# Kernel tuning notes

Measured on AMD Instinct MI355X. Metric: run time of the kernel, lower is better.

Reference implementation:

```python
import jax, jax.numpy as jnp
import numpy as np

DIM = 1024
DIM_HEAD = 64
S = 8   # num_searches
R = 2   # num_retrievals
B = 2
N = 2048


def setup_inputs() -> dict:
    key = jax.random.key(0)
    ks = jax.random.split(key, 7)
    wscale = 1.0 / np.sqrt(DIM)
    return {
        "x": jax.random.normal(ks[0], (B, N, DIM), dtype=jnp.float32),
        "Wsq": jax.random.normal(ks[1], (DIM, S * DIM_HEAD), dtype=jnp.float32) * wscale,
        "Wsk": jax.random.normal(ks[2], (DIM, S * DIM_HEAD), dtype=jnp.float32) * wscale,
        "Wrv": jax.random.normal(ks[3], (DIM, R * DIM_HEAD), dtype=jnp.float32) * wscale,
        "Wrq": jax.random.normal(ks[4], (DIM, S * DIM_HEAD), dtype=jnp.float32) * wscale,
        "Wrk": jax.random.normal(ks[5], (DIM_HEAD, DIM_HEAD), dtype=jnp.float32) * (1.0 / np.sqrt(DIM_HEAD)),
        "Wout": jax.random.normal(ks[6], (S * DIM_HEAD, DIM), dtype=jnp.float32) * (1.0 / np.sqrt(S * DIM_HEAD)),
    }


def reference(x, Wsq, Wsk, Wrv, Wrq, Wrk, Wout):
    b, n, _ = x.shape
    d = DIM_HEAD
    scale = d ** -0.5

    # search queries/keys: [b, s, n, d]
    sq = (x @ Wsq).reshape(b, n, S, d).transpose(0, 2, 1, 3)
    sk = (x @ Wsk).reshape(b, n, S, d).transpose(0, 2, 1, 3)

    # search attention over sequence: [b, s, n, n]
    sim = jnp.einsum('bsid,bsjd->bsij', sq, sk) * scale
    attn = jax.nn.softmax(sim, axis=-1)

    # retrieval values: [b, r, n, d]
    v = (x @ Wrv).reshape(b, n, R, d).transpose(0, 2, 1, 3)

    # each search retrieves with every retrieval value set: [b, s, r, n, d]
    retrieved = jnp.einsum('bsij,brjd->bsrid', attn, v)

    # retrieval queries [b, s, n, d] and transformed retrieval keys [b, s, r, n, d]
    rq = (x @ Wrq).reshape(b, n, S, d).transpose(0, 2, 1, 3)
    rk = jnp.einsum('bsrnd,de->bsrne', retrieved, Wrk)

    # compositional softmax over retrievals: [b, s, n, r]
    r_sim = jnp.einsum('bsnd,bsrnd->bsnr', rq, rk) * scale
    r_attn = jax.nn.softmax(r_sim, axis=-1)

    # combine: [b, s, n, d] -> [b, n, s*d]
    out = jnp.einsum('bsnr,bsrnd->bsnd', r_attn, retrieved)
    out = out.transpose(0, 2, 1, 3).reshape(b, n, S * d)
    return out @ Wout
```

## Files before the change

### kernel.cpp

```cpp
#include <hip/hip_runtime.h>

#define NSEQ 2048
#define KDIM 1024
#define DH   64
#define NS   8
#define NR   2

typedef short bf16x8 __attribute__((ext_vector_type(8)));
typedef float f32x4  __attribute__((ext_vector_type(4)));

typedef unsigned short ushort_ma __attribute__((may_alias));
typedef bf16x8         bf16x8_ma __attribute__((may_alias));
typedef uint4          uint4_ma  __attribute__((may_alias));
typedef uint2          uint2_ma  __attribute__((may_alias));
typedef float4         float4_ma __attribute__((may_alias));

__device__ __forceinline__ unsigned short f2bf(float f) {
    unsigned int u = __builtin_bit_cast(unsigned int, f);
    u = (u + 0x7FFFu + ((u >> 16) & 1u)) >> 16;
    return (unsigned short)u;
}
__device__ __forceinline__ float bf2f(unsigned short h) {
    unsigned int u = ((unsigned int)h) << 16;
    return __builtin_bit_cast(float, u);
}
__device__ __forceinline__ unsigned int cvt_pk_bf16(float lo, float hi) {
    unsigned int r;
    asm("v_cvt_pk_bf16_f32 %0, %1, %2" : "=v"(r) : "v"(lo), "v"(hi));
    return r;
}
__device__ __forceinline__ float exp2_raw(float x) {
    return __builtin_amdgcn_exp2f(x);
}
__device__ __forceinline__ void gld_lds16(void* lptr, const void* gptr) {
    __builtin_amdgcn_global_load_lds(
        (const __attribute__((address_space(1))) unsigned int*)gptr,
        (__attribute__((address_space(3))) unsigned int*)lptr, 16, 0, 0);
}

__global__ __launch_bounds__(256) void prep_all_k(
    const float* __restrict__ Wsq, const float* __restrict__ Wsk,
    const float* __restrict__ Wrq, const float* __restrict__ Wrv,
    const float* __restrict__ Wout, const float* __restrict__ Wrk,
    const float* __restrict__ x,
    unsigned short* __restrict__ Wt, unsigned short* __restrict__ Wot,
    unsigned short* __restrict__ xh)
{
    __shared__ float sBuf[2][64][65];
    const int tid = threadIdx.x;
    const int bid = blockIdx.x;

    if (bid >= 672) {
        const int total = 4096 * KDIM / 4;
        int idx = (bid - 672) * 256 + tid;
        for (int i = idx; i < total; i += 2048 * 256) {
            float4 v = ((const float4_ma*)x)[i];
            ushort4 h;
            h.x = f2bf(v.x); h.y = f2bf(v.y); h.z = f2bf(v.z); h.w = f2bf(v.w);
            ((ushort4*)xh)[i] = h;
        }
        return;
    }

    if (bid >= 544) {
        const int r = bid - 544;
        const int s = r & 7;
        const int k0 = (r >> 3) * 64;
        float (*sQ)[65] = sBuf[0];
        float (*sK)[65] = sBuf[1];
#pragma unroll
        for (int p = 0; p < 4; ++p) {
            int row = (tid >> 4) + p * 16;
            int col = (tid & 15) * 4;
            float4 w = *(const float4*)&Wrk[(size_t)row * 64 + col];
            sK[row][col + 0] = w.x; sK[row][col + 1] = w.y;
            sK[row][col + 2] = w.z; sK[row][col + 3] = w.w;
            float4 q = *(const float4*)&Wrq[(size_t)(k0 + row) * 512 + s * 64 + col];
            sQ[row][col + 0] = q.x; sQ[row][col + 1] = q.y;
            sQ[row][col + 2] = q.z; sQ[row][col + 3] = q.w;
        }
        __syncthreads();

        const int dd = tid >> 2;
        const int kq = (tid & 3) * 16;
        float acc[16];
#pragma unroll
        for (int j = 0; j < 16; ++j) acc[j] = 0.f;
        for (int e = 0; e < 64; ++e) {
            float w = sK[dd][e];
#pragma unroll
            for (int j = 0; j < 16; ++j) acc[j] += w * sQ[kq + j][e];
        }
        const float SC = 0.125f * 1.44269504089f;
        unsigned int w8[8];
#pragma unroll
        for (int j = 0; j < 8; ++j)
            w8[j] = (unsigned)f2bf(acc[2 * j] * SC) | ((unsigned)f2bf(acc[2 * j + 1] * SC) << 16);
        unsigned short* o = Wt + (size_t)(1024 + s * 64 + dd) * KDIM + k0 + kq;
        *(uint4_ma*)o       = make_uint4(w8[0], w8[1], w8[2], w8[3]);
        *(uint4_ma*)(o + 8) = make_uint4(w8[4], w8[5], w8[6], w8[7]);
        return;
    }

    {
        const float* src; int ldw, k0, n0, scol, ldo;
        unsigned short* dst;
        float sc = 1.0f;
        if (bid < 416) {
            int kt = bid / 26, nt = bid % 26;
            k0 = kt * 64; n0 = nt * 64;
            if (n0 >= 1024 && n0 < 1536) return;
            if (n0 < 512)       { src = Wsq; ldw = 512; scol = n0;        sc = 0.125f * 1.44269504089f; }
            else if (n0 < 1024) { src = Wsk; ldw = 512; scol = n0 - 512;  }
            else                { src = Wrv; ldw = 128; scol = n0 - 1536; }
            dst = Wt; ldo = KDIM;
        } else {
            int r = bid - 416;
            int kt = r >> 4, nt = r & 15;
            k0 = kt * 64; n0 = nt * 64; scol = n0;
            src = Wout; ldw = KDIM;
            dst = Wot; ldo = 512;
        }
        float (*sT)[65] = sBuf[0];
#pragma unroll
        for (int p = 0; p < 4; ++p) {
            int row = (tid >> 4) + p * 16;
            int col = (tid & 15) * 4;
            float4 v = *(const float4*)&src[(size_t)(k0 + row) * ldw + scol + col];
            sT[row][col + 0] = v.x; sT[row][col + 1] = v.y;
            sT[row][col + 2] = v.z; sT[row][col + 3] = v.w;
        }
        __syncthreads();

        int n_l = tid >> 2, kg = (tid & 3) * 16;
        unsigned int w[8];
#pragma unroll
        for (int j = 0; j < 8; ++j) {
            unsigned short a = f2bf(sT[kg + 2 * j][n_l] * sc);
            unsigned short b = f2bf(sT[kg + 2 * j + 1][n_l] * sc);
            w[j] = (unsigned)a | ((unsigned)b << 16);
        }
        unsigned short* o = dst + (size_t)(n0 + n_l) * ldo + k0 + kg;
        *(uint4_ma*)o       = make_uint4(w[0], w[1], w[2], w[3]);
        *(uint4_ma*)(o + 8) = make_uint4(w[4], w[5], w[6], w[7]);
    }
}

__global__ __launch_bounds__(256) void proj_mfma_k(
    const unsigned short* __restrict__ xh,
    const unsigned short* __restrict__ Wt,
    unsigned short* __restrict__ Qb, unsigned short* __restrict__ Kf,
    unsigned short* __restrict__ RUb, unsigned short* __restrict__ Vf)
{
    __shared__ __align__(16) char smem[32768];
    const int tid = threadIdx.x;
    const int bn = blockIdx.x, bm = blockIdx.y;
    const int wid = tid >> 6, lane = tid & 63;
    const int wm = wid >> 1, wn = wid & 1;
    const int lrow = lane & 15, lgrp = lane >> 4;
    const int lr = lane >> 3, lc = lane & 7;

    f32x4 acc[4][4];
#pragma unroll
    for (int i = 0; i < 4; ++i)
#pragma unroll
        for (int j = 0; j < 4; ++j) acc[i][j] = (f32x4){0.f, 0.f, 0.f, 0.f};

    for (int kt = 0; kt < KDIM / 64; ++kt) {
        __syncthreads();
#pragma unroll
        for (int i = 0; i < 4; ++i) {
            int seg = wid * 4 + i;
            int r = seg * 8 + lr;
            gld_lds16(smem + seg * 1024,
                      xh + (size_t)(bm * 128 + r) * KDIM + kt * 64 + (lc ^ (r & 7)) * 8);
            gld_lds16(smem + 16384 + seg * 1024,
                      Wt + (size_t)(bn * 128 + r) * KDIM + kt * 64 + (lc ^ (r & 7)) * 8);
        }
        __syncthreads();
#pragma unroll
        for (int ks = 0; ks < 2; ++ks) {
            bf16x8 bfr[4];
#pragma unroll
            for (int nf = 0; nf < 4; ++nf) {
                int rb = wn * 64 + nf * 16 + lrow;
                bfr[nf] = *(bf16x8_ma*)(smem + 16384 + ((rb * 128 + ks * 64 + lgrp * 16) ^ ((rb & 7) << 4)));
            }
#pragma unroll
            for (int mf = 0; mf < 4; ++mf) {
                int ra = wm * 64 + mf * 16 + lrow;
                bf16x8 ah = *(bf16x8_ma*)(smem + ((ra * 128 + ks * 64 + lgrp * 16) ^ ((ra & 7) << 4)));
#pragma unroll
                for (int nf = 0; nf < 4; ++nf)
                    acc[mf][nf] = __builtin_amdgcn_mfma_f32_16x16x32_bf16(ah, bfr[nf], acc[mf][nf], 0, 0, 0);
            }
        }
    }

    const int g = bn >> 2;
#pragma unroll
    for (int mf = 0; mf < 4; ++mf) {
#pragma unroll
        for (int nf = 0; nf < 4; ++nf) {
            int j0 = bn * 128 + wn * 64 + nf * 16 + lrow;
            int m0 = bm * 128 + wm * 64 + mf * 16 + lgrp * 4;
            if (g == 3) {
                int dv = j0 - 1536;
                int bb = m0 >> 11, seq = m0 & (NSEQ - 1);
                size_t addr = (size_t)bb * 262144 + (size_t)(seq >> 6) * 8192
                    + (size_t)(((dv >> 4) * 2 + ((seq >> 5) & 1)) * 512)
                    + (((seq >> 3) & 3) * 16 + (dv & 15)) * 8 + (seq & 7);
                ushort4 h;
                h.x = f2bf(acc[mf][nf][0]); h.y = f2bf(acc[mf][nf][1]);
                h.z = f2bf(acc[mf][nf][2]); h.w = f2bf(acc[mf][nf][3]);
                *(ushort4*)&Vf[addr] = h;
            } else if (g == 1) {
                int s = (j0 >> 6) & 7, d = j0 & 63;
#pragma unroll
                for (int r = 0; r < 4; ++r) {
                    int m = m0 + r;
                    int bb = m >> 11, seq = m & (NSEQ - 1);
                    size_t base = ((size_t)(bb * NS + s)) * (NSEQ * DH)
                        + (size_t)(seq >> 6) * 4096
                        + ((((seq >> 4) & 3) * 2 + (d >> 5)) * 64
                           + ((d & 31) >> 3) * 16 + (seq & 15)) * 8 + (d & 7);
                    Kf[base] = f2bf(acc[mf][nf][r]);
                }
            } else {
                int s = (j0 >> 6) & 7, d = j0 & 63;
                unsigned short* basep = (g == 0) ? Qb : RUb;
#pragma unroll
                for (int r = 0; r < 4; ++r) {
                    int m = m0 + r;
                    int bb = m >> 11, seq = m & (NSEQ - 1);
                    basep[(((size_t)(bb * NS + s)) * NSEQ + seq) * DH + d] = f2bf(acc[mf][nf][r]);
                }
            }
        }
    }
}

__global__ __launch_bounds__(256) void attn_mfma_k(
    const unsigned short* __restrict__ Qb, const unsigned short* __restrict__ Kfr,
    const unsigned short* __restrict__ Vfr, const unsigned short* __restrict__ RUb,
    unsigned short* __restrict__ O1b)
{
    __shared__ __align__(16) char smem[8192];
    const int tid = threadIdx.x;
    const int gblk = blockIdx.x;
    const int orig = ((gblk & 7) << 6) + (gblk >> 3);
    const int qt = orig & 31, s = (orig >> 5) & 7, b = orig >> 8;
    const int wid = tid >> 6, lane = tid & 63;
    const int lrow = lane & 15, lgrp = lane >> 4;

    const unsigned short* Qg = Qb + (((size_t)(b * NS + s)) * NSEQ + qt * 64) * DH;
    const unsigned short* kp0 = Kfr + ((size_t)(b * NS + s)) * (NSEQ * DH) + lane * 8;
    const unsigned short* kp1 = kp0 + 2048;
    const unsigned short* vp0 = Vfr + (size_t)b * 262144 + lane * 8;
    const unsigned short* vp1 = vp0 + 2048;
    const unsigned short* vp2 = vp0 + 4096;
    const unsigned short* vp3 = vp0 + 6144;

    bf16x8 qf[2];
    {
        const unsigned short* qrow = Qg + (wid * 16 + lrow) * DH + lgrp * 8;
        qf[0] = *(const bf16x8_ma*)(qrow);
        qf[1] = *(const bf16x8_ma*)(qrow + 32);
    }

    char* sPw = smem + wid * 2048;
    const int pswz = (lrow & 7) << 4;

    bf16x8 kf[8], vf[16];
#define LOADK() do {                                                          \
        kf[0] = *(const bf16x8_ma*)(kp0);                                     \
        kf[1] = *(const bf16x8_ma*)(kp0 + 512);                               \
        kf[2] = *(const bf16x8_ma*)(kp0 + 1024);                              \
        kf[3] = *(const bf16x8_ma*)(kp0 + 1536);                              \
        kf[4] = *(const bf16x8_ma*)(kp1);                                     \
        kf[5] = *(const bf16x8_ma*)(kp1 + 512);                               \
        kf[6] = *(const bf16x8_ma*)(kp1 + 1024);                              \
        kf[7] = *(const bf16x8_ma*)(kp1 + 1536);                              \
        kp0 += 4096; kp1 += 4096;                                             \
    } while (0)
#define LOADV() do {                                                          \
        _Pragma("unroll")                                                     \
        for (int i_ = 0; i_ < 4; ++i_) {                                      \
            vf[i_]      = *(const bf16x8_ma*)(vp0 + i_ * 512);                \
            vf[4 + i_]  = *(const bf16x8_ma*)(vp1 + i_ * 512);                \
            vf[8 + i_]  = *(const bf16x8_ma*)(vp2 + i_ * 512);                \
            vf[12 + i_] = *(const bf16x8_ma*)(vp3 + i_ * 512);                \
        }                                                                     \
        vp0 += 8192; vp1 += 8192; vp2 += 8192; vp3 += 8192;                   \
    } while (0)

    f32x4 oacc[8];
#pragma unroll
    for (int df = 0; df < 8; ++df) oacc[df] = (f32x4){0.f, 0.f, 0.f, 0.f};
    float l_ = 0.f;
    f32x4 st[4];

    const int NT = NSEQ / 64;
    LOADK();

    for (int t = 0; t < NT; ++t) {
        LOADV();

        __builtin_amdgcn_s_setprio(1);
#pragma unroll
        for (int nf = 0; nf < 4; ++nf) {
            st[nf] = (f32x4){0.f, 0.f, 0.f, 0.f};
            st[nf] = __builtin_amdgcn_mfma_f32_16x16x32_bf16(kf[nf * 2],     qf[0], st[nf], 0, 0, 0);
            st[nf] = __builtin_amdgcn_mfma_f32_16x16x32_bf16(kf[nf * 2 + 1], qf[1], st[nf], 0, 0, 0);
        }
        __builtin_amdgcn_s_setprio(0);

        LOADK();

        float rs = 0.f;
#pragma unroll
        for (int nf = 0; nf < 4; ++nf)
#pragma unroll
            for (int r = 0; r < 4; ++r) {
                float p = exp2_raw(st[nf][r]);
                st[nf][r] = p;
                rs += p;
            }
        l_ += rs;

#pragma unroll
        for (int nf = 0; nf < 4; ++nf) {
            uint2 w;
            w.x = cvt_pk_bf16(st[nf][0], st[nf][1]);
            w.y = cvt_pk_bf16(st[nf][2], st[nf][3]);
            *(uint2_ma*)(sPw + ((lrow * 128 + nf * 32 + lgrp * 8) ^ pswz)) = w;
        }

        __builtin_amdgcn_s_setprio(1);
#pragma unroll
        for (int kkv = 0; kkv < 2; ++kkv) {
            bf16x8 pf = *(bf16x8_ma*)(sPw + ((lrow * 128 + kkv * 64 + lgrp * 16) ^ pswz));
#pragma unroll
            for (int df = 0; df < 8; ++df)
                oacc[df] = __builtin_amdgcn_mfma_f32_16x16x32_bf16(vf[df * 2 + kkv], pf, oacc[df], 0, 0, 0);
        }
        __builtin_amdgcn_s_setprio(0);
    }
#undef LOADK
#undef LOADV

    l_ += __shfl_xor(l_, 16);
    l_ += __shfl_xor(l_, 32);

    {
        const int n = qt * 64 + wid * 16 + lrow;
        const unsigned short* ug = RUb + ((((size_t)(b * NS + s)) * NSEQ) + n) * DH + lgrp * 4;
        float s0 = 0.f, s1 = 0.f;
#pragma unroll
        for (int df = 0; df < 4; ++df) {
            ushort4 u4 = *(const ushort4*)(ug + df * 16);
            float ux = bf2f(u4.x), uy = bf2f(u4.y), uz = bf2f(u4.z), uw = bf2f(u4.w);
            s0 += oacc[df][0] * ux + oacc[df][1] * uy + oacc[df][2] * uz + oacc[df][3] * uw;
            s1 += oacc[df + 4][0] * ux + oacc[df + 4][1] * uy + oacc[df + 4][2] * uz + oacc[df + 4][3] * uw;
        }
        s0 += __shfl_xor(s0, 16); s0 += __shfl_xor(s0, 32);
        s1 += __shfl_xor(s1, 16); s1 += __shfl_xor(s1, 32);
        float invl = 1.f / l_;
        float r0v = s0 * invl, r1v = s1 * invl;
        float mm = fmaxf(r0v, r1v);
        float e0 = exp2_raw(r0v - mm), e1 = exp2_raw(r1v - mm);
        float w = invl / (e0 + e1);
        float a0 = e0 * w, a1 = e1 * w;

        unsigned short* dst = O1b + ((size_t)(b * NSEQ + n)) * (NS * DH) + s * DH + lgrp * 4;
#pragma unroll
        for (int df = 0; df < 4; ++df) {
            float c0 = a0 * oacc[df][0] + a1 * oacc[df + 4][0];
            float c1 = a0 * oacc[df][1] + a1 * oacc[df + 4][1];
            float c2 = a0 * oacc[df][2] + a1 * oacc[df + 4][2];
            float c3 = a0 * oacc[df][3] + a1 * oacc[df + 4][3];
            uint2 o2;
            o2.x = cvt_pk_bf16(c0, c1);
            o2.y = cvt_pk_bf16(c2, c3);
            *(uint2_ma*)(dst + df * 16) = o2;
        }
    }
}

__global__ __launch_bounds__(256) void out_mfma_k(
    const unsigned short* __restrict__ A, const unsigned short* __restrict__ Bw,
    float* __restrict__ C)
{
    __shared__ __align__(16) char smem[32768];
    const int tid = threadIdx.x;
    const int bn = blockIdx.x, bm = blockIdx.y;
    const int wid = tid >> 6, lane = tid & 63;
    const int wm = wid >> 1, wn = wid & 1;
    const int lrow = lane & 15, lgrp = lane >> 4;
    const int lr = lane >> 3, lc = lane & 7;
    const int KD = NS * DH;

    f32x4 acc[4][4];
#pragma unroll
    for (int i = 0; i < 4; ++i)
#pragma unroll
        for (int j = 0; j < 4; ++j) acc[i][j] = (f32x4){0.f, 0.f, 0.f, 0.f};

    for (int kt = 0; kt < KD / 64; ++kt) {
        __syncthreads();
#pragma unroll
        for (int i = 0; i < 4; ++i) {
            int seg = wid * 4 + i;
            int r = seg * 8 + lr;
            gld_lds16(smem + seg * 1024,
                      A + (size_t)(bm * 128 + r) * KD + kt * 64 + (lc ^ (r & 7)) * 8);
            gld_lds16(smem + 16384 + seg * 1024,
                      Bw + (size_t)(bn * 128 + r) * KD + kt * 64 + (lc ^ (r & 7)) * 8);
        }
        __syncthreads();
#pragma unroll
        for (int ks = 0; ks < 2; ++ks) {
            bf16x8 bfr[4];
#pragma unroll
            for (int nf = 0; nf < 4; ++nf) {
                int rb = wn * 64 + nf * 16 + lrow;
                bfr[nf] = *(bf16x8_ma*)(smem + 16384 + ((rb * 128 + ks * 64 + lgrp * 16) ^ ((rb & 7) << 4)));
            }
#pragma unroll
            for (int mf = 0; mf < 4; ++mf) {
                int ra = wm * 64 + mf * 16 + lrow;
                bf16x8 af = *(bf16x8_ma*)(smem + ((ra * 128 + ks * 64 + lgrp * 16) ^ ((ra & 7) << 4)));
#pragma unroll
                for (int nf = 0; nf < 4; ++nf)
                    acc[mf][nf] = __builtin_amdgcn_mfma_f32_16x16x32_bf16(af, bfr[nf], acc[mf][nf], 0, 0, 0);
            }
        }
    }

#pragma unroll
    for (int mf = 0; mf < 4; ++mf) {
#pragma unroll
        for (int nf = 0; nf < 4; ++nf) {
            int j0 = bn * 128 + wn * 64 + nf * 16 + lrow;
            int m0 = bm * 128 + wm * 64 + mf * 16 + lgrp * 4;
#pragma unroll
            for (int r = 0; r < 4; ++r)
                C[(size_t)(m0 + r) * KDIM + j0] = acc[mf][nf][r];
        }
    }
}

extern "C" void kernel_launch(void* const* d_in, const int* in_sizes, int n_in,
                              void* d_out, int out_size, void* d_ws, size_t ws_size,
                              hipStream_t stream)
{
    const float* x    = (const float*)d_in[0];
    const float* Wsq  = (const float*)d_in[1];
    const float* Wsk  = (const float*)d_in[2];
    const float* Wrv  = (const float*)d_in[3];
    const float* Wrq  = (const float*)d_in[4];
    const float* Wrk  = (const float*)d_in[5];
    const float* Wout = (const float*)d_in[6];
    float* out = (float*)d_out;

    unsigned short* RUb  = (unsigned short*)d_ws;
    unsigned short* Wt   = RUb + (size_t)2 * NS * NSEQ * DH;
    unsigned short* Wot  = Wt + (size_t)1664 * KDIM;
    unsigned short* Qb   = Wot + (size_t)KDIM * 512;
    unsigned short* Kfr  = Qb + (size_t)2 * NS * NSEQ * DH;
    unsigned short* Vfr  = Kfr + (size_t)2 * NS * NSEQ * DH;
    unsigned short* xh   = Vfr + (size_t)2 * 128 * NSEQ;
    unsigned short* O1b  = xh;

    prep_all_k<<<2720, 256, 0, stream>>>(Wsq, Wsk, Wrq, Wrv, Wout, Wrk, x, Wt, Wot, xh);
    proj_mfma_k<<<dim3(13, 32), 256, 0, stream>>>(xh, Wt, Qb, Kfr, RUb, Vfr);
    attn_mfma_k<<<512, 256, 0, stream>>>(Qb, Kfr, Vfr, RUb, O1b);
    out_mfma_k<<<dim3(8, 32), 256, 0, stream>>>(O1b, Wot, out);
}
```

Before: 107.0 us.

## Prefetch K and V tiles with inline-asm global loads and manual vmcnt waits

Replaces the compiler-generated K/V fragment loads in the attention loop with inline-asm global_load_dwordx4 and explicit s_waitcnt vmcnt counters. V for the next tile is now issued right after the PV MFMAs, so the V fetch overlaps the following QK MFMAs and softmax instead of stalling at the start of each tile. Sched barriers pin the ordering. The risk is that asm volatile loads hide dependencies from the compiler, and any wrong vmcnt count gives a data race. The extra in-flight registers may also lower occupancy.

```diff
diff --git a/kernel.cpp b/kernel.cpp
--- a/kernel.cpp
+++ b/kernel.cpp
@@ -272,27 +272,40 @@
     const int pswz = (lrow & 7) << 4;
 
     bf16x8 kf[8], vf[16];
-#define LOADK() do {                                                          \
-        kf[0] = *(const bf16x8_ma*)(kp0);                                     \
-        kf[1] = *(const bf16x8_ma*)(kp0 + 512);                               \
-        kf[2] = *(const bf16x8_ma*)(kp0 + 1024);                              \
-        kf[3] = *(const bf16x8_ma*)(kp0 + 1536);                              \
-        kf[4] = *(const bf16x8_ma*)(kp1);                                     \
-        kf[5] = *(const bf16x8_ma*)(kp1 + 512);                               \
-        kf[6] = *(const bf16x8_ma*)(kp1 + 1024);                              \
-        kf[7] = *(const bf16x8_ma*)(kp1 + 1536);                              \
-        kp0 += 4096; kp1 += 4096;                                             \
-    } while (0)
-#define LOADV() do {                                                          \
-        _Pragma("unroll")                                                     \
-        for (int i_ = 0; i_ < 4; ++i_) {                                      \
-            vf[i_]      = *(const bf16x8_ma*)(vp0 + i_ * 512);                \
-            vf[4 + i_]  = *(const bf16x8_ma*)(vp1 + i_ * 512);                \
-            vf[8 + i_]  = *(const bf16x8_ma*)(vp2 + i_ * 512);                \
-            vf[12 + i_] = *(const bf16x8_ma*)(vp3 + i_ * 512);                \
-        }                                                                     \
-        vp0 += 8192; vp1 += 8192; vp2 += 8192; vp3 += 8192;                   \
-    } while (0)
+#define LOADK_ASM() do {                                                              \
+    asm volatile("global_load_dwordx4 %0, %1, off"             : "=&v"(kf[0]) : "v"(kp0)); \
+    asm volatile("global_load_dwordx4 %0, %1, off offset:1024" : "=&v"(kf[1]) : "v"(kp0)); \
+    asm volatile("global_load_dwordx4 %0, %1, off offset:2048" : "=&v"(kf[2]) : "v"(kp0)); \
+    asm volatile("global_load_dwordx4 %0, %1, off offset:3072" : "=&v"(kf[3]) : "v"(kp0)); \
+    asm volatile("global_load_dwordx4 %0, %1, off"             : "=&v"(kf[4]) : "v"(kp1)); \
+    asm volatile("global_load_dwordx4 %0, %1, off offset:1024" : "=&v"(kf[5]) : "v"(kp1)); \
+    asm volatile("global_load_dwordx4 %0, %1, off offset:2048" : "=&v"(kf[6]) : "v"(kp1)); \
+    asm volatile("global_load_dwordx4 %0, %1, off offset:3072" : "=&v"(kf[7]) : "v"(kp1)); \
+    kp0 += 4096; kp1 += 4096;                                                         \
+} while (0)
+#define LOADV_ASM() do {                                                              \
+    asm volatile("global_load_dwordx4 %0, %1, off"             : "=&v"(vf[0])  : "v"(vp0)); \
+    asm volatile("global_load_dwordx4 %0, %1, off offset:1024" : "=&v"(vf[1])  : "v"(vp0)); \
+    asm volatile("global_load_dwordx4 %0, %1, off offset:2048" : "=&v"(vf[2])  : "v"(vp0)); \
+    asm volatile("global_load_dwordx4 %0, %1, off offset:3072" : "=&v"(vf[3])  : "v"(vp0)); \
+    asm volatile("global_load_dwordx4 %0, %1, off"             : "=&v"(vf[4])  : "v"(vp1)); \
+    asm volatile("global_load_dwordx4 %0, %1, off offset:1024" : "=&v"(vf[5])  : "v"(vp1)); \
+    asm volatile("global_load_dwordx4 %0, %1, off offset:2048" : "=&v"(vf[6])  : "v"(vp1)); \
+    asm volatile("global_load_dwordx4 %0, %1, off offset:3072" : "=&v"(vf[7])  : "v"(vp1)); \
+    asm volatile("global_load_dwordx4 %0, %1, off"             : "=&v"(vf[8])  : "v"(vp2)); \
+    asm volatile("global_load_dwordx4 %0, %1, off offset:1024" : "=&v"(vf[9])  : "v"(vp2)); \
+    asm volatile("global_load_dwordx4 %0, %1, off offset:2048" : "=&v"(vf[10]) : "v"(vp2)); \
+    asm volatile("global_load_dwordx4 %0, %1, off offset:3072" : "=&v"(vf[11]) : "v"(vp2)); \
+    asm volatile("global_load_dwordx4 %0, %1, off"             : "=&v"(vf[12]) : "v"(vp3)); \
+    asm volatile("global_load_dwordx4 %0, %1, off offset:1024" : "=&v"(vf[13]) : "v"(vp3)); \
+    asm volatile("global_load_dwordx4 %0, %1, off offset:2048" : "=&v"(vf[14]) : "v"(vp3)); \
+    asm volatile("global_load_dwordx4 %0, %1, off offset:3072" : "=&v"(vf[15]) : "v"(vp3)); \
+    vp0 += 8192; vp1 += 8192; vp2 += 8192; vp3 += 8192;                               \
+} while (0)
+#define WAITCNT(N) do {                                                       \
+    asm volatile("s_waitcnt vmcnt(" #N ")" ::: "memory");                     \
+    __builtin_amdgcn_sched_barrier(0);                                        \
+} while (0)
 
     f32x4 oacc[8];
 #pragma unroll
@@ -301,10 +314,11 @@
     f32x4 st[4];
 
     const int NT = NSEQ / 64;
-    LOADK();
+    LOADK_ASM();
+    LOADV_ASM();
 
     for (int t = 0; t < NT; ++t) {
-        LOADV();
+        WAITCNT(16);
 
         __builtin_amdgcn_s_setprio(1);
 #pragma unroll
@@ -315,7 +329,7 @@
         }
         __builtin_amdgcn_s_setprio(0);
 
-        LOADK();
+        LOADK_ASM();
 
         float rs = 0.f;
 #pragma unroll
@@ -336,6 +350,8 @@
             *(uint2_ma*)(sPw + ((lrow * 128 + nf * 32 + lgrp * 8) ^ pswz)) = w;
         }
 
+        WAITCNT(8);
+
         __builtin_amdgcn_s_setprio(1);
 #pragma unroll
         for (int kkv = 0; kkv < 2; ++kkv) {
@@ -345,9 +361,14 @@
                 oacc[df] = __builtin_amdgcn_mfma_f32_16x16x32_bf16(vf[df * 2 + kkv], pf, oacc[df], 0, 0, 0);
         }
         __builtin_amdgcn_s_setprio(0);
-    }
-#undef LOADK
-#undef LOADV
+
+        LOADV_ASM();
+    }
+    asm volatile("s_waitcnt vmcnt(0)" ::: "memory");
+    __builtin_amdgcn_sched_barrier(0);
+#undef LOADK_ASM
+#undef LOADV_ASM
+#undef WAITCNT
 
     l_ += __shfl_xor(l_, 16);
     l_ += __shfl_xor(l_, 32);
```

Result: no change. 106.3 us (-0.7%).
